# Performance work log

Hardware: AMD Instinct MI355X
Metric: run time of the kernel (lower is better)

The kernel has to match this reference:

```python
import jax, jax.numpy as jnp
import numpy as np


def gcn_conv(x, edge_index, edge_weight, W, b):
    """PyG GCNConv: add self-loops (weight 1), symmetric degree norm, aggregate, linear."""
    N = x.shape[0]
    loop = jnp.arange(N, dtype=edge_index.dtype)
    src = jnp.concatenate([edge_index[0], loop])
    dst = jnp.concatenate([edge_index[1], loop])
    ew = jnp.concatenate([edge_weight, jnp.ones((N,), dtype=x.dtype)])
    deg = jax.ops.segment_sum(ew, dst, num_segments=N)
    dinv = jnp.where(deg > 0, jax.lax.rsqrt(deg), 0.0)
    norm = dinv[src] * ew * dinv[dst]            # [E+N]
    h = x @ W                                    # [N, out] transform first
    msg = h[src] * norm[:, None]                 # gather + scale
    out = jax.ops.segment_sum(msg, dst, num_segments=N)  # scatter-add
    return out + b


def l2norm(x, eps=1e-12):
    n = jnp.sqrt(jnp.sum(x * x, axis=-1, keepdims=True))
    return x / jnp.maximum(n, eps)


def setup_inputs() -> dict:
    key = jax.random.key(0)
    ks = jax.random.split(key, 16)
    N_net, E_net, N_dag, E_dag = 100000, 600000, 50000, 400000
    D_net, D_dag, H_net, H_dag = 128, 128, 128, 128
    s = lambda fan_in: 1.0 / np.sqrt(fan_in)
    return {
        "net_feat": jax.random.normal(ks[0], (N_net, D_net), jnp.float32),
        "net_edge_index": jax.random.randint(ks[1], (2, E_net), 0, N_net, jnp.int32),
        "net_edge_weights": jax.random.uniform(ks[2], (E_net,), jnp.float32),
        "dag_feat": jax.random.normal(ks[3], (N_dag, D_dag), jnp.float32),
        "dag_edge_index": jax.random.randint(ks[4], (2, E_dag), 0, N_dag, jnp.int32),
        "dag_edge_weights": jax.random.uniform(ks[5], (E_dag,), jnp.float32),
        "W_net": jax.random.normal(ks[6], (D_net, H_net), jnp.float32) * s(D_net),
        "b_net": jnp.zeros((H_net,), jnp.float32),
        "W_dag": jax.random.normal(ks[7], (D_dag, H_dag), jnp.float32) * s(D_dag),
        "b_dag": jnp.zeros((H_dag,), jnp.float32),
        "W1": jax.random.normal(ks[8], (H_net + H_dag, 64), jnp.float32) * s(H_net + H_dag),
        "b1": jnp.zeros((64,), jnp.float32),
        "W2": jax.random.normal(ks[9], (64, 1), jnp.float32) * s(64),
        "b2": jnp.zeros((1,), jnp.float32),
    }


def reference(net_feat, net_edge_index, net_edge_weights,
              dag_feat, dag_edge_index, dag_edge_weights,
              W_net, b_net, W_dag, b_dag, W1, b1, W2, b2):
    net_emb = jax.nn.relu(gcn_conv(net_feat, net_edge_index, net_edge_weights, W_net, b_net))
    dag_emb = jax.nn.relu(gcn_conv(dag_feat, dag_edge_index, dag_edge_weights, W_dag, b_dag))
    # normalize == True
    net_emb = l2norm(net_emb)
    dag_emb = l2norm(dag_emb)
    # net_batch/dag_batch are None: mean over nodes -> single state value
    net_vec = net_emb.mean(axis=0)
    dag_vec = dag_emb.mean(axis=0)
    combined = jnp.concatenate([net_vec, dag_vec], axis=-1)
    h = jax.nn.relu(combined @ W1 + b1)
    state_val = h @ W2 + b2
    return state_val
```

## Files before the change

kernel.cpp:

```cpp
#include <hip/hip_runtime.h>

#define FD 128
#define PAD 48
#define WSCALE 16777216.0f
#define WINV   5.9604645e-8f
#define GGRID 768

typedef __attribute__((ext_vector_type(8))) short short8;
typedef __attribute__((ext_vector_type(4))) float f32x4;

__device__ inline unsigned short f2bf(float f) {
    unsigned u = __float_as_uint(f);
    return (unsigned short)((u + 0x7fffu + ((u >> 16) & 1u)) >> 16);
}
__device__ inline void bf4_to_f32(uint2 u, float& a, float& b, float& c, float& d) {
    a = __uint_as_float(u.x << 16);
    b = __uint_as_float(u.x & 0xffff0000u);
    c = __uint_as_float(u.y << 16);
    d = __uint_as_float(u.y & 0xffff0000u);
}
__device__ inline float pc_to_dinv(unsigned long long pv) {
    return rsqrtf((float)(pv & 0xffffffffull) * WINV + 1.0f);
}
__device__ inline void split1(float x, unsigned short& h, unsigned short& l) {
    unsigned u = __float_as_uint(x);
    unsigned hh = (u + 0x7fffu + ((u >> 16) & 1u)) >> 16;
    float r = x - __uint_as_float(hh << 16);
    unsigned u2 = __float_as_uint(r);
    h = (unsigned short)hh;
    l = (unsigned short)((u2 + 0x7fffu + ((u2 >> 16) & 1u)) >> 16);
}
__device__ __forceinline__ void gl_lds4(const void* g, void* l) {
    __builtin_amdgcn_global_load_lds(
        (const __attribute__((address_space(1))) unsigned int*)g,
        (__attribute__((address_space(3))) unsigned int*)l, 4, 0, 0);
}

__global__ __launch_bounds__(256) void bucket_pack(
        const int* __restrict__ ei_n, const float* __restrict__ ew_n,
        unsigned long long* __restrict__ pc_n, int2* __restrict__ el_n,
        int E_n, int GBn,
        const int* __restrict__ ei_d, const float* __restrict__ ew_d,
        unsigned long long* __restrict__ pc_d, int2* __restrict__ el_d,
        int E_d,
        const float* __restrict__ Wn, const float* __restrict__ Wd,
        unsigned short* __restrict__ Wpack) {
    int b = blockIdx.x;
    int packStart = (int)gridDim.x - 16;
    if (b >= packStart) {
        int p = b - packStart;
        int graph = p >> 3, pb = p & 7;
        const float* W = graph ? Wd : Wn;
        int c  = threadIdx.x & 127;
        int hh = threadIdx.x >> 7;
        int k0 = pb * 16 + hh * 8;
        short8 hv, lv;
        #pragma unroll
        for (int j = 0; j < 8; j++) {
            unsigned short hq, lq;
            split1(W[(k0 + j) * FD + c], hq, lq);
            hv[j] = (short)hq; lv[j] = (short)lq;
        }
        char* dst = (char*)Wpack + graph * 65536
                  + c * 256 + 16 * ((k0 >> 3) ^ (c & 15));
        *(short8*)dst = hv;
        *(short8*)(dst + 32768) = lv;
        return;
    }
    const int* ei; const float* ew; unsigned long long* pc; int2* el; int E, e;
    if (b < GBn) { ei = ei_n; ew = ew_n; pc = pc_n; el = el_n; E = E_n;
                   e = b * 256 + threadIdx.x; }
    else         { ei = ei_d; ew = ew_d; pc = pc_d; el = el_d; E = E_d;
                   e = (b - GBn) * 256 + threadIdx.x; }
    if (e < E) {
        int src = ei[e];
        int dst = ei[E + e];
        float w = ew[e];
        unsigned long long val =
            (1ull << 32) |
            (unsigned long long)(unsigned int)__float2uint_rn(w * WSCALE);
        unsigned long long old = atomicAdd(&pc[dst], val);
        unsigned int pos = (unsigned int)(old >> 32);
        if (pos < PAD)
            el[(size_t)dst * PAD + pos] = make_int2(src, __float_as_int(w));
    }
}

__global__ __launch_bounds__(256) void gemm_mfma(
        const float* __restrict__ X_n, const unsigned long long* __restrict__ pc_n,
        unsigned short* __restrict__ hs_n, int N_n, int Gn,
        const float* __restrict__ X_d, const unsigned long long* __restrict__ pc_d,
        unsigned short* __restrict__ hs_d, int N_d,
        const unsigned short* __restrict__ Wpack) {
    __shared__ unsigned short WL[2][128][128];

    const float* X; const unsigned long long* pc; unsigned short* hs; int N, r0;
    const char* wsrc;
    if (blockIdx.x < Gn) { X = X_n; pc = pc_n; hs = hs_n; N = N_n;
                           r0 = blockIdx.x * 128; wsrc = (const char*)Wpack; }
    else                 { X = X_d; pc = pc_d; hs = hs_d; N = N_d;
                           r0 = (blockIdx.x - Gn) * 128;
                           wsrc = (const char*)Wpack + 65536; }

    const int tid  = threadIdx.x;
    const int w    = tid >> 6;
    const int lane = tid & 63;
    const int c15  = lane & 15;
    const int g    = lane >> 4;

    {
        const float4* s4 = (const float4*)wsrc;
        float4* d4 = (float4*)WL;
        #pragma unroll
        for (int i = 0; i < 16; i++) d4[tid + i * 256] = s4[tid + i * 256];
    }
    __syncthreads();

    f32x4 acc[2][8] = {};

    const int row0 = r0 + 32 * w + c15;
    const float* x0p = X + (size_t)row0 * FD;
    const float* x1p = x0p + 16 * FD;
    const bool v0 = row0 < N, v1 = (row0 + 16) < N;

    #pragma unroll
    for (int kt = 0; kt < 4; kt++) {
        const int ko = 32 * kt + 8 * g;
        float4 a0 = {}, a1 = {}, c0 = {}, c1 = {};
        if (v0) { a0 = *(const float4*)(x0p + ko); c0 = *(const float4*)(x0p + ko + 4); }
        if (v1) { a1 = *(const float4*)(x1p + ko); c1 = *(const float4*)(x1p + ko + 4); }
        short8 ah0, al0, ah1, al1;
        {
            float xx[8] = {a0.x, a0.y, a0.z, a0.w, c0.x, c0.y, c0.z, c0.w};
            #pragma unroll
            for (int j = 0; j < 8; j++) {
                unsigned short hq, lq; split1(xx[j], hq, lq);
                ah0[j] = (short)hq; al0[j] = (short)lq;
            }
        }
        {
            float xx[8] = {a1.x, a1.y, a1.z, a1.w, c1.x, c1.y, c1.z, c1.w};
            #pragma unroll
            for (int j = 0; j < 8; j++) {
                unsigned short hq, lq; split1(xx[j], hq, lq);
                ah1[j] = (short)hq; al1[j] = (short)lq;
            }
        }

        const char* bbase = (const char*)WL + c15 * 256
                          + 16 * (((unsigned)(g + 4 * kt)) ^ (unsigned)c15);
        #pragma unroll
        for (int cf = 0; cf < 8; cf++) {
            short8 bh = *(const short8*)(bbase + cf * 4096);
            short8 bl = *(const short8*)(bbase + cf * 4096 + 32768);
            acc[0][cf] = __builtin_amdgcn_mfma_f32_16x16x32_bf16(ah0, bh, acc[0][cf], 0, 0, 0);
            acc[1][cf] = __builtin_amdgcn_mfma_f32_16x16x32_bf16(ah1, bh, acc[1][cf], 0, 0, 0);
            acc[0][cf] = __builtin_amdgcn_mfma_f32_16x16x32_bf16(al0, bh, acc[0][cf], 0, 0, 0);
            acc[1][cf] = __builtin_amdgcn_mfma_f32_16x16x32_bf16(al1, bh, acc[1][cf], 0, 0, 0);
            acc[0][cf] = __builtin_amdgcn_mfma_f32_16x16x32_bf16(ah0, bl, acc[0][cf], 0, 0, 0);
            acc[1][cf] = __builtin_amdgcn_mfma_f32_16x16x32_bf16(ah1, bl, acc[1][cf], 0, 0, 0);
        }
    }

    __syncthreads();
    unsigned short* OT = (unsigned short*)WL;
    #pragma unroll
    for (int rf = 0; rf < 2; rf++) {
        float dv[4];
        #pragma unroll
        for (int r = 0; r < 4; r++) {
            int row = r0 + 32 * w + 16 * rf + 4 * g + r;
            dv[r] = pc_to_dinv(row < N ? pc[row] : 0ull);
        }
        #pragma unroll
        for (int cf = 0; cf < 8; cf++) {
            #pragma unroll
            for (int r = 0; r < 4; r++) {
                int lrow = 32 * w + 16 * rf + 4 * g + r;
                unsigned byteo = (unsigned)(lrow * 256)
                               + (unsigned)((32 * cf + 2 * c15) ^ ((lrow & 15) << 4));
                *(unsigned short*)((char*)OT + byteo) = f2bf(acc[rf][cf][r] * dv[r]);
            }
        }
    }
    __syncthreads();
    #pragma unroll
    for (int p = 0; p < 8; p++) {
        int idx  = p * 256 + tid;
        int lrow = idx >> 4, ch = idx & 15;
        int row  = r0 + lrow;
        if (row < N) {
            uint4 v = *(const uint4*)((const char*)WL + lrow * 256
                                      + 16 * (ch ^ (lrow & 15)));
            *(uint4*)&hs[(size_t)row * FD + ch * 8] = v;
        }
    }
}

__global__ __launch_bounds__(256) void gather_reduce_both(
        const unsigned short* __restrict__ hs_n,
        const unsigned long long* __restrict__ pc_n, const int2* __restrict__ el_n,
        const float* __restrict__ b_n, int N_n,
        const unsigned short* __restrict__ hs_d,
        const unsigned long long* __restrict__ pc_d, const int2* __restrict__ el_d,
        const float* __restrict__ b_d, int N_d,
        float* __restrict__ vec) {
    __shared__ char ring[4][2][12][512];

    const int tid  = threadIdx.x;
    const int wv   = tid >> 6;
    const int lane = tid & 63;
    const int h    = lane >> 5;
    const int sl   = lane & 31;
    const int hw   = tid >> 5;

    const int loff = (sl < 16) ? (h * 128 + sl * 8) : (256 + h * 128 + (sl - 16) * 8);
    const int fo   = (sl < 16) ? (sl * 4) : (64 + (sl - 16) * 4);

    float4 bbn = *(const float4*)&b_n[fo];
    float4 bbd = *(const float4*)&b_d[fo];
    float an0 = 0.f, an1 = 0.f, an2 = 0.f, an3 = 0.f;
    float ad0 = 0.f, ad1 = 0.f, ad2 = 0.f, ad3 = 0.f;

    const int total = N_n + N_d;
    const int S     = GGRID * 8;
    const int t0    = blockIdx.x * 8 + hw;
    const int tA0   = blockIdx.x * 8 + 2 * wv;
    const int nIter = (total - tA0 + S - 1) / S;

    struct Meta {
        unsigned long long pv;
        int2 my;
        uint2 self;
        const unsigned short* hs;
        const int2* el;
        int i, isn, valid;
    };

    auto loadMeta = [&](int t) {
        Meta m;
        m.valid = (t < total);
        int tt = m.valid ? t : 0;
        m.isn = (tt < N_n);
        int i = m.isn ? tt : tt - N_n;
        m.i  = i;
        m.hs = m.isn ? hs_n : hs_d;
        m.el = (m.isn ? el_n : el_d) + (size_t)i * PAD;
        m.pv = (m.isn ? pc_n : pc_d)[i];
        m.my = (sl < 16) ? m.el[sl] : make_int2(0, 0);
        m.self = *(const uint2*)(m.hs + (size_t)i * FD + fo);
        return m;
    };

    auto issueEdges = [&](const Meta& m, char* buf) {
        int cn = (int)(m.pv >> 32); if (cn > PAD) cn = PAD;
        const char* base = (const char*)m.hs;
        #pragma unroll
        for (int u = 0; u < 12; u++) {
            int q  = __shfl(m.my.x, u, 32);
            int qq = (u < cn) ? q : m.i;
            const char* g = base + (size_t)qq * 256 + sl * 4;
            gl_lds4(g,       buf + u * 512);
            gl_lds4(g + 128, buf + u * 512 + 256);
        }
    };

    auto consume = [&](const Meta& m, const char* buf) {
        int cnt = (int)(m.pv >> 32); if (cnt > PAD) cnt = PAD;
        const float dv = pc_to_dinv(m.pv);
        float s0, s1, s2, s3; bf4_to_f32(m.self, s0, s1, s2, s3);
        float x0 = s0 * dv, x1 = s1 * dv, x2 = s2 * dv, x3 = s3 * dv;
        #pragma unroll
        for (int u = 0; u < 12; u++) {
            uint2 e = *(const uint2*)(buf + u * 512 + loff);
            int wi = __shfl(m.my.y, u, 32);
            float w = (u < cnt) ? __int_as_float(wi) * dv : 0.f;
            float a, b2, c, d; bf4_to_f32(e, a, b2, c, d);
            x0 = fmaf(a, w, x0); x1 = fmaf(b2, w, x1);
            x2 = fmaf(c, w, x2); x3 = fmaf(d, w, x3);
        }
        if (__any(cnt > 12)) {
            #pragma unroll
            for (int u = 12; u < 16; u++) {
                int q  = __shfl(m.my.x, u, 32);
                int wi = __shfl(m.my.y, u, 32);
                bool act = (u < cnt);
                float w = act ? __int_as_float(wi) * dv : 0.f;
                int qq = act ? q : m.i;
                uint2 e = *(const uint2*)((const char*)m.hs + (size_t)qq * 256 + fo * 2);
                float a, b2, c, d; bf4_to_f32(e, a, b2, c, d);
                x0 = fmaf(a, w, x0); x1 = fmaf(b2, w, x1);
                x2 = fmaf(c, w, x2); x3 = fmaf(d, w, x3);
            }
            if (__any(cnt > 16)) {
                for (int j = 16; j < cnt; j++) {
                    int2 p = m.el[j];
                    float w = __int_as_float(p.y) * dv;
                    uint2 e = *(const uint2*)((const char*)m.hs + (size_t)p.x * 256 + fo * 2);
                    float a, b2, c, d; bf4_to_f32(e, a, b2, c, d);
                    x0 = fmaf(a, w, x0); x1 = fmaf(b2, w, x1);
                    x2 = fmaf(c, w, x2); x3 = fmaf(d, w, x3);
                }
            }
        }
        float4 bb = m.isn ? bbn : bbd;
        x0 = fmaxf(x0 + bb.x, 0.f);
        x1 = fmaxf(x1 + bb.y, 0.f);
        x2 = fmaxf(x2 + bb.z, 0.f);
        x3 = fmaxf(x3 + bb.w, 0.f);
        float ss = fmaf(x0, x0, fmaf(x1, x1, fmaf(x2, x2, x3 * x3)));
        #pragma unroll
        for (int o = 16; o; o >>= 1) ss += __shfl_xor(ss, o);
        float inv = 1.0f / fmaxf(sqrtf(ss), 1e-12f);
        inv = m.valid ? inv : 0.f;
        if (m.isn) {
            an0 = fmaf(x0, inv, an0); an1 = fmaf(x1, inv, an1);
            an2 = fmaf(x2, inv, an2); an3 = fmaf(x3, inv, an3);
        } else {
            ad0 = fmaf(x0, inv, ad0); ad1 = fmaf(x1, inv, ad1);
            ad2 = fmaf(x2, inv, ad2); ad3 = fmaf(x3, inv, ad3);
        }
    };

    char* cur = &ring[wv][0][0][0];
    char* nxt = &ring[wv][1][0][0];

    Meta m0 = loadMeta(t0);
    Meta m1 = loadMeta(t0 + S);
    issueEdges(m0, cur);

    for (int it = 0; it < nIter; ++it) {
        Meta m2 = loadMeta(t0 + (it + 2) * S);
        issueEdges(m1, nxt);
        asm volatile("s_waitcnt vmcnt(27)" ::: "memory");
        __builtin_amdgcn_sched_barrier(0);
        consume(m0, cur);
        m0 = m1; m1 = m2;
        char* tmp = cur; cur = nxt; nxt = tmp;
    }

    asm volatile("s_waitcnt vmcnt(0)" ::: "memory");
    __syncthreads();
    float* accw = (float*)ring;
    accw[hw * 256 + fo + 0] = an0;
    accw[hw * 256 + fo + 1] = an1;
    accw[hw * 256 + fo + 2] = an2;
    accw[hw * 256 + fo + 3] = an3;
    accw[hw * 256 + 128 + fo + 0] = ad0;
    accw[hw * 256 + 128 + fo + 1] = ad1;
    accw[hw * 256 + 128 + fo + 2] = ad2;
    accw[hw * 256 + 128 + fo + 3] = ad3;
    __syncthreads();
    {
        float s = accw[0 * 256 + tid] + accw[1 * 256 + tid]
                + accw[2 * 256 + tid] + accw[3 * 256 + tid]
                + accw[4 * 256 + tid] + accw[5 * 256 + tid]
                + accw[6 * 256 + tid] + accw[7 * 256 + tid];
        unsafeAtomicAdd(&vec[tid], s);
    }
}

__global__ __launch_bounds__(256) void final_kernel(
        const float* __restrict__ vec,
        const float* __restrict__ W1, const float* __restrict__ b1,
        const float* __restrict__ W2, const float* __restrict__ b2,
        float* __restrict__ out, float invNnet, float invNdag) {
    __shared__ float part[4][64];
    int j = threadIdx.x & 63;
    int q = threadIdx.x >> 6;
    float h = 0.f;
    for (int k = q * 64; k < q * 64 + 64; k++) {
        float sc = (k < 128) ? invNnet : invNdag;
        h = fmaf(vec[k] * sc, W1[k * 64 + j], h);
    }
    part[q][j] = h;
    __syncthreads();
    if (threadIdx.x < 64) {
        float hh = b1[j] + part[0][j] + part[1][j] + part[2][j] + part[3][j];
        hh = fmaxf(hh, 0.f);
        float p = hh * W2[j];
        #pragma unroll
        for (int o = 32; o; o >>= 1) p += __shfl_xor(p, o);
        if (j == 0) out[0] = p + b2[0];
    }
}

extern "C" void kernel_launch(void* const* d_in, const int* in_sizes, int n_in,
                              void* d_out, int out_size, void* d_ws, size_t ws_size,
                              hipStream_t stream) {
    const float* net_feat = (const float*)d_in[0];
    const int*   net_ei   = (const int*)d_in[1];
    const float* net_ew   = (const float*)d_in[2];
    const float* dag_feat = (const float*)d_in[3];
    const int*   dag_ei   = (const int*)d_in[4];
    const float* dag_ew   = (const float*)d_in[5];
    const float* W_net    = (const float*)d_in[6];
    const float* b_net    = (const float*)d_in[7];
    const float* W_dag    = (const float*)d_in[8];
    const float* b_dag    = (const float*)d_in[9];
    const float* W1       = (const float*)d_in[10];
    const float* b1       = (const float*)d_in[11];
    const float* W2       = (const float*)d_in[12];
    const float* b2       = (const float*)d_in[13];

    const int N_net = in_sizes[0] / FD;
    const int E_net = in_sizes[2];
    const int N_dag = in_sizes[3] / FD;
    const int E_dag = in_sizes[5];
    const int GBn = (E_net + 255) / 256, GBd = (E_dag + 255) / 256;
    const int Gn  = (N_net + 127) / 128, Gd  = (N_dag + 127) / 128;

    char* w = (char*)d_ws;
    size_t o = 0;
    unsigned short* hs_net = (unsigned short*)(w + o); o += (size_t)2 * N_net * FD;
    unsigned short* hs_dag = (unsigned short*)(w + o); o += (size_t)2 * N_dag * FD;
    unsigned long long* pc_net = (unsigned long long*)(w + o); o += (size_t)8 * N_net;
    unsigned long long* pc_dag = (unsigned long long*)(w + o); o += (size_t)8 * N_dag;
    float* vec = (float*)(w + o); o += 256 * 4;
    size_t zbytes = (size_t)8 * (N_net + N_dag) + 256 * 4;
    int2* elist_net = (int2*)(w + o); o += (size_t)8 * N_net * PAD;
    int2* elist_dag = (int2*)(w + o); o += (size_t)8 * N_dag * PAD;
    unsigned short* Wpack = (unsigned short*)(w + o); o += 131072;

    hipMemsetAsync(pc_net, 0, zbytes, stream);

    bucket_pack<<<GBn + GBd + 16, 256, 0, stream>>>(
        net_ei, net_ew, pc_net, elist_net, E_net, GBn,
        dag_ei, dag_ew, pc_dag, elist_dag, E_dag,
        W_net, W_dag, Wpack);

    gemm_mfma<<<Gn + Gd, 256, 0, stream>>>(
        net_feat, pc_net, hs_net, N_net, Gn,
        dag_feat, pc_dag, hs_dag, N_dag, Wpack);

    gather_reduce_both<<<GGRID, 256, 0, stream>>>(
        hs_net, pc_net, elist_net, b_net, N_net,
        hs_dag, pc_dag, elist_dag, b_dag, N_dag, vec);

    final_kernel<<<1, 256, 0, stream>>>(vec, W1, b1, W2, b2, (float*)d_out,
                                        1.0f / (float)N_net, 1.0f / (float)N_dag);
}
```

Before: 316.9 us.

## Use 16-byte global-to-LDS loads and unified buffers in gather kernel

Replaces the 4-byte global_load_lds calls with 16-byte ones, so each wave fetches two nodes' neighbor rows in 6 wide issues instead of 24 narrow ones. The wait count drops from 27 to 9 to match. It also treats the net and dag arrays as one contiguous buffer indexed by a row offset, which removes per-node pointer selection, and uses packed float2 FMAs for the accumulation. This relies on hs, pc and elist for the two graphs being laid out back to back in the workspace, and changes the feature mapping for each lane to contiguous sl*4.

After: 313.6 us. About the same (-1.0%).

```diff
diff --git a/kernel.cpp b/kernel.cpp
--- a/kernel.cpp
+++ b/kernel.cpp
@@ -8,16 +8,11 @@
 
 typedef __attribute__((ext_vector_type(8))) short short8;
 typedef __attribute__((ext_vector_type(4))) float f32x4;
+typedef __attribute__((ext_vector_type(2))) float f32x2;
 
 __device__ inline unsigned short f2bf(float f) {
     unsigned u = __float_as_uint(f);
     return (unsigned short)((u + 0x7fffu + ((u >> 16) & 1u)) >> 16);
-}
-__device__ inline void bf4_to_f32(uint2 u, float& a, float& b, float& c, float& d) {
-    a = __uint_as_float(u.x << 16);
-    b = __uint_as_float(u.x & 0xffff0000u);
-    c = __uint_as_float(u.y << 16);
-    d = __uint_as_float(u.y & 0xffff0000u);
 }
 __device__ inline float pc_to_dinv(unsigned long long pv) {
     return rsqrtf((float)(pv & 0xffffffffull) * WINV + 1.0f);
@@ -30,10 +25,10 @@
     h = (unsigned short)hh;
     l = (unsigned short)((u2 + 0x7fffu + ((u2 >> 16) & 1u)) >> 16);
 }
-__device__ __forceinline__ void gl_lds4(const void* g, void* l) {
+__device__ __forceinline__ void gl_lds16(const void* g, void* l) {
     __builtin_amdgcn_global_load_lds(
         (const __attribute__((address_space(1))) unsigned int*)g,
-        (__attribute__((address_space(3))) unsigned int*)l, 4, 0, 0);
+        (__attribute__((address_space(3))) unsigned int*)l, 16, 0, 0);
 }
 
 __global__ __launch_bounds__(256) void bucket_pack(
@@ -198,14 +193,12 @@
 }
 
 __global__ __launch_bounds__(256) void gather_reduce_both(
-        const unsigned short* __restrict__ hs_n,
-        const unsigned long long* __restrict__ pc_n, const int2* __restrict__ el_n,
-        const float* __restrict__ b_n, int N_n,
-        const unsigned short* __restrict__ hs_d,
-        const unsigned long long* __restrict__ pc_d, const int2* __restrict__ el_d,
-        const float* __restrict__ b_d, int N_d,
-        float* __restrict__ vec) {
-    __shared__ char ring[4][2][12][512];
+        const unsigned short* __restrict__ hs_all,
+        const unsigned long long* __restrict__ pc_all,
+        const int2* __restrict__ el_all,
+        const float* __restrict__ b_n, const float* __restrict__ b_d,
+        int N_n, int N_d, float* __restrict__ vec) {
+    __shared__ __align__(16) char ring[4][2][6][1024];
 
     const int tid  = threadIdx.x;
     const int wv   = tid >> 6;
@@ -213,14 +206,14 @@
     const int h    = lane >> 5;
     const int sl   = lane & 31;
     const int hw   = tid >> 5;
-
-    const int loff = (sl < 16) ? (h * 128 + sl * 8) : (256 + h * 128 + (sl - 16) * 8);
-    const int fo   = (sl < 16) ? (sl * 4) : (64 + (sl - 16) * 4);
-
-    float4 bbn = *(const float4*)&b_n[fo];
-    float4 bbd = *(const float4*)&b_d[fo];
-    float an0 = 0.f, an1 = 0.f, an2 = 0.f, an3 = 0.f;
-    float ad0 = 0.f, ad1 = 0.f, ad2 = 0.f, ad3 = 0.f;
+    const char* hsb = (const char*)hs_all;
+
+    float4 bn4 = *(const float4*)&b_n[sl * 4];
+    float4 bd4 = *(const float4*)&b_d[sl * 4];
+    f32x2 bbn01 = {bn4.x, bn4.y}, bbn23 = {bn4.z, bn4.w};
+    f32x2 bbd01 = {bd4.x, bd4.y}, bbd23 = {bd4.z, bd4.w};
+    f32x2 an01 = {0.f, 0.f}, an23 = {0.f, 0.f};
+    f32x2 ad01 = {0.f, 0.f}, ad23 = {0.f, 0.f};
 
     const int total = N_n + N_d;
     const int S     = GGRID * 8;
@@ -232,9 +225,7 @@
         unsigned long long pv;
         int2 my;
         uint2 self;
-        const unsigned short* hs;
-        const int2* el;
-        int i, isn, valid;
+        int row, eb, isn, valid;
     };
 
     auto loadMeta = [&](int t) {
@@ -242,42 +233,54 @@
         m.valid = (t < total);
         int tt = m.valid ? t : 0;
         m.isn = (tt < N_n);
-        int i = m.isn ? tt : tt - N_n;
-        m.i  = i;
-        m.hs = m.isn ? hs_n : hs_d;
-        m.el = (m.isn ? el_n : el_d) + (size_t)i * PAD;
-        m.pv = (m.isn ? pc_n : pc_d)[i];
-        m.my = (sl < 16) ? m.el[sl] : make_int2(0, 0);
-        m.self = *(const uint2*)(m.hs + (size_t)i * FD + fo);
+        m.row = tt;
+        m.eb  = m.isn ? 0 : N_n;
+        m.pv  = pc_all[tt];
+        m.my  = (sl < 16) ? el_all[(size_t)tt * PAD + sl] : make_int2(0, 0);
+        m.self = *(const uint2*)(hsb + (size_t)tt * 256 + sl * 8);
         return m;
     };
 
+    const int node   = (lane >> 4) & 1;
+    const int ub     = lane >> 5;
+    const int rowoff = (lane & 15) * 16;
+
     auto issueEdges = [&](const Meta& m, char* buf) {
         int cn = (int)(m.pv >> 32); if (cn > PAD) cn = PAD;
-        const char* base = (const char*)m.hs;
-        #pragma unroll
-        for (int u = 0; u < 12; u++) {
-            int q  = __shfl(m.my.x, u, 32);
-            int qq = (u < cn) ? q : m.i;
-            const char* g = base + (size_t)qq * 256 + sl * 4;
-            gl_lds4(g,       buf + u * 512);
-            gl_lds4(g + 128, buf + u * 512 + 256);
+        int cnN  = __shfl(cn,    node * 32, 64);
+        int rowN = __shfl(m.row, node * 32, 64);
+        int ebN  = __shfl(m.eb,  node * 32, 64);
+        #pragma unroll
+        for (int p = 0; p < 6; p++) {
+            int u  = 2 * p + ub;
+            int q  = __shfl(m.my.x, node * 32 + u, 64);
+            int qq = (u < cnN) ? (q + ebN) : rowN;
+            unsigned off = (unsigned)qq * 256u + rowoff;
+            gl_lds16(hsb + off, buf + p * 1024);
         }
     };
 
     auto consume = [&](const Meta& m, const char* buf) {
         int cnt = (int)(m.pv >> 32); if (cnt > PAD) cnt = PAD;
         const float dv = pc_to_dinv(m.pv);
-        float s0, s1, s2, s3; bf4_to_f32(m.self, s0, s1, s2, s3);
-        float x0 = s0 * dv, x1 = s1 * dv, x2 = s2 * dv, x3 = s3 * dv;
+        f32x2 dvv = {dv, dv};
+        f32x2 s01 = {__uint_as_float(m.self.x << 16),
+                     __uint_as_float(m.self.x & 0xffff0000u)};
+        f32x2 s23 = {__uint_as_float(m.self.y << 16),
+                     __uint_as_float(m.self.y & 0xffff0000u)};
+        f32x2 x01 = s01 * dvv;
+        f32x2 x23 = s23 * dvv;
+        const char* cbase = buf + h * 256 + sl * 8;
         #pragma unroll
         for (int u = 0; u < 12; u++) {
-            uint2 e = *(const uint2*)(buf + u * 512 + loff);
+            uint2 e = *(const uint2*)(cbase + u * 512);
             int wi = __shfl(m.my.y, u, 32);
             float w = (u < cnt) ? __int_as_float(wi) * dv : 0.f;
-            float a, b2, c, d; bf4_to_f32(e, a, b2, c, d);
-            x0 = fmaf(a, w, x0); x1 = fmaf(b2, w, x1);
-            x2 = fmaf(c, w, x2); x3 = fmaf(d, w, x3);
+            f32x2 ww = {w, w};
+            f32x2 p01 = {__uint_as_float(e.x << 16), __uint_as_float(e.x & 0xffff0000u)};
+            f32x2 p23 = {__uint_as_float(e.y << 16), __uint_as_float(e.y & 0xffff0000u)};
+            x01 = __builtin_elementwise_fma(p01, ww, x01);
+            x23 = __builtin_elementwise_fma(p23, ww, x23);
         }
         if (__any(cnt > 12)) {
             #pragma unroll
@@ -286,70 +289,76 @@
                 int wi = __shfl(m.my.y, u, 32);
                 bool act = (u < cnt);
                 float w = act ? __int_as_float(wi) * dv : 0.f;
-                int qq = act ? q : m.i;
-                uint2 e = *(const uint2*)((const char*)m.hs + (size_t)qq * 256 + fo * 2);
-                float a, b2, c, d; bf4_to_f32(e, a, b2, c, d);
-                x0 = fmaf(a, w, x0); x1 = fmaf(b2, w, x1);
-                x2 = fmaf(c, w, x2); x3 = fmaf(d, w, x3);
+                int qq = act ? (q + m.eb) : m.row;
+                uint2 e = *(const uint2*)(hsb + (size_t)qq * 256 + sl * 8);
+                f32x2 ww = {w, w};
+                f32x2 p01 = {__uint_as_float(e.x << 16), __uint_as_float(e.x & 0xffff0000u)};
+                f32x2 p23 = {__uint_as_float(e.y << 16), __uint_as_float(e.y & 0xffff0000u)};
+                x01 = __builtin_elementwise_fma(p01, ww, x01);
+                x23 = __builtin_elementwise_fma(p23, ww, x23);
             }
             if (__any(cnt > 16)) {
                 for (int j = 16; j < cnt; j++) {
-                    int2 p = m.el[j];
-                    float w = __int_as_float(p.y) * dv;
-                    uint2 e = *(const uint2*)((const char*)m.hs + (size_t)p.x * 256 + fo * 2);
-                    float a, b2, c, d; bf4_to_f32(e, a, b2, c, d);
-                    x0 = fmaf(a, w, x0); x1 = fmaf(b2, w, x1);
-                    x2 = fmaf(c, w, x2); x3 = fmaf(d, w, x3);
+                    int2 pe = el_all[(size_t)m.row * PAD + j];
+                    float w = __int_as_float(pe.y) * dv;
+                    uint2 e = *(const uint2*)(hsb + (size_t)(pe.x + m.eb) * 256 + sl * 8);
+                    f32x2 ww = {w, w};
+                    f32x2 p01 = {__uint_as_float(e.x << 16), __uint_as_float(e.x & 0xffff0000u)};
+                    f32x2 p23 = {__uint_as_float(e.y << 16), __uint_as_float(e.y & 0xffff0000u)};
+                    x01 = __builtin_elementwise_fma(p01, ww, x01);
+                    x23 = __builtin_elementwise_fma(p23, ww, x23);
                 }
             }
         }
-        float4 bb = m.isn ? bbn : bbd;
-        x0 = fmaxf(x0 + bb.x, 0.f);
-        x1 = fmaxf(x1 + bb.y, 0.f);
-        x2 = fmaxf(x2 + bb.z, 0.f);
-        x3 = fmaxf(x3 + bb.w, 0.f);
-        float ss = fmaf(x0, x0, fmaf(x1, x1, fmaf(x2, x2, x3 * x3)));
+        f32x2 zero = {0.f, 0.f};
+        f32x2 bb01 = m.isn ? bbn01 : bbd01;
+        f32x2 bb23 = m.isn ? bbn23 : bbd23;
+        x01 = __builtin_elementwise_max(x01 + bb01, zero);
+        x23 = __builtin_elementwise_max(x23 + bb23, zero);
+        float ss = fmaf(x01.x, x01.x, fmaf(x01.y, x01.y,
+                   fmaf(x23.x, x23.x, x23.y * x23.y)));
         #pragma unroll
         for (int o = 16; o; o >>= 1) ss += __shfl_xor(ss, o);
         float inv = 1.0f / fmaxf(sqrtf(ss), 1e-12f);
-        inv = m.valid ? inv : 0.f;
-        if (m.isn) {
-            an0 = fmaf(x0, inv, an0); an1 = fmaf(x1, inv, an1);
-            an2 = fmaf(x2, inv, an2); an3 = fmaf(x3, inv, an3);
-        } else {
-            ad0 = fmaf(x0, inv, ad0); ad1 = fmaf(x1, inv, ad1);
-            ad2 = fmaf(x2, inv, ad2); ad3 = fmaf(x3, inv, ad3);
-        }
+        float gn = (m.valid && m.isn)  ? inv : 0.f;
+        float gd = (m.valid && !m.isn) ? inv : 0.f;
+        f32x2 gn2 = {gn, gn}, gd2 = {gd, gd};
+        an01 = __builtin_elementwise_fma(x01, gn2, an01);
+        an23 = __builtin_elementwise_fma(x23, gn2, an23);
+        ad01 = __builtin_elementwise_fma(x01, gd2, ad01);
+        ad23 = __builtin_elementwise_fma(x23, gd2, ad23);
     };
 
     char* cur = &ring[wv][0][0][0];
     char* nxt = &ring[wv][1][0][0];
 
-    Meta m0 = loadMeta(t0);
-    Meta m1 = loadMeta(t0 + S);
-    issueEdges(m0, cur);
-
-    for (int it = 0; it < nIter; ++it) {
-        Meta m2 = loadMeta(t0 + (it + 2) * S);
-        issueEdges(m1, nxt);
-        asm volatile("s_waitcnt vmcnt(27)" ::: "memory");
-        __builtin_amdgcn_sched_barrier(0);
-        consume(m0, cur);
-        m0 = m1; m1 = m2;
-        char* tmp = cur; cur = nxt; nxt = tmp;
+    if (nIter > 0) {
+        Meta m0 = loadMeta(t0);
+        Meta m1 = loadMeta(t0 + S);
+        issueEdges(m0, cur);
+
+        for (int it = 0; it < nIter; ++it) {
+            Meta m2 = loadMeta(t0 + (it + 2) * S);
+            issueEdges(m1, nxt);
+            asm volatile("s_waitcnt vmcnt(9)" ::: "memory");
+            __builtin_amdgcn_sched_barrier(0);
+            consume(m0, cur);
+            m0 = m1; m1 = m2;
+            char* tmp = cur; cur = nxt; nxt = tmp;
+        }
     }
 
     asm volatile("s_waitcnt vmcnt(0)" ::: "memory");
     __syncthreads();
     float* accw = (float*)ring;
-    accw[hw * 256 + fo + 0] = an0;
-    accw[hw * 256 + fo + 1] = an1;
-    accw[hw * 256 + fo + 2] = an2;
-    accw[hw * 256 + fo + 3] = an3;
-    accw[hw * 256 + 128 + fo + 0] = ad0;
-    accw[hw * 256 + 128 + fo + 1] = ad1;
-    accw[hw * 256 + 128 + fo + 2] = ad2;
-    accw[hw * 256 + 128 + fo + 3] = ad3;
+    accw[hw * 256 + sl * 4 + 0] = an01.x;
+    accw[hw * 256 + sl * 4 + 1] = an01.y;
+    accw[hw * 256 + sl * 4 + 2] = an23.x;
+    accw[hw * 256 + sl * 4 + 3] = an23.y;
+    accw[hw * 256 + 128 + sl * 4 + 0] = ad01.x;
+    accw[hw * 256 + 128 + sl * 4 + 1] = ad01.y;
+    accw[hw * 256 + 128 + sl * 4 + 2] = ad23.x;
+    accw[hw * 256 + 128 + sl * 4 + 3] = ad23.y;
     __syncthreads();
     {
         float s = accw[0 * 256 + tid] + accw[1 * 256 + tid]
@@ -434,8 +443,7 @@
         dag_feat, pc_dag, hs_dag, N_dag, Wpack);
 
     gather_reduce_both<<<GGRID, 256, 0, stream>>>(
-        hs_net, pc_net, elist_net, b_net, N_net,
-        hs_dag, pc_dag, elist_dag, b_dag, N_dag, vec);
+        hs_net, pc_net, elist_net, b_net, b_dag, N_net, N_dag, vec);
 
     final_kernel<<<1, 256, 0, stream>>>(vec, W1, b1, W2, b2, (float*)d_out,
                                         1.0f / (float)N_net, 1.0f / (float)N_dag);
```
